# Kernel tuning notes

Measured on AMD Instinct MI355X. Metric: run time of the kernel, lower is better.

## Reference

```python
import jax, jax.numpy as jnp
import numpy as np

# Wong-Wang-Deco neural mass parameters (whobpyt defaults)
G=20.0; LAMBDA=0.0; A_E=310.0; B_E=125.0; D_E=0.16; TAU_E=100.0; W_E=1.0
A_I=615.0; B_I=177.0; D_I=0.087; TAU_I=10.0; W_I=0.7
W_PLUS=1.4; J_NMDA=0.15; J=1.0; GAMMA=0.641e-3; GAMMA_I=1.0e-3
SIG=0.01; I_0=0.382; I_EXT=0.0
DT=0.0001  # step_size
N_REGIONS=512; N_STEPS=20000


def _H(I, a, b, d, big_c):
    # firing-rate transfer function H_for_*_V3
    x = a * I - b
    numer = jnp.abs(x) + 1e-9
    neg = -d * x
    denom = jnp.where(
        neg > 50.0,
        jnp.abs(1.0 - big_c * neg) + 1e-9 * d,
        jnp.abs(1.0 - jnp.exp(jnp.minimum(neg, 51.0))) + 1e-9 * d,
    )
    return numer / denom


def setup_inputs() -> dict:
    key = jax.random.key(0)
    k1, k2, k3 = jax.random.split(key, 3)
    init_state = jax.random.uniform(k1, (N_REGIONS, 2), dtype=jnp.float32) * 0.2
    # row-normalized random structural connectivity
    Con_Mtx = jax.random.uniform(k2, (N_REGIONS, N_REGIONS), dtype=jnp.float32) / N_REGIONS
    v_of_T = jax.random.normal(k3, (N_STEPS, N_REGIONS), dtype=jnp.float32)
    return {"init_state": init_state, "Con_Mtx": Con_Mtx, "v_of_T": v_of_T}


def reference(init_state, Con_Mtx, v_of_T):
    S_E0 = init_state[:, 0]
    S_I0 = init_state[:, 1]

    def step(carry, v):
        S_E, S_I = carry
        Network_S_E = Con_Mtx @ S_E  # [N]
        I_E = W_E * I_0 + W_PLUS * J_NMDA * S_E + G * J_NMDA * Network_S_E - J * S_I + I_EXT
        I_I = W_I * I_0 + J_NMDA * S_E - S_I + LAMBDA * G * J_NMDA * Network_S_E
        r_E = _H(I_E, A_E, B_E, D_E, 1e9)
        r_I = _H(I_I, A_I, B_I, D_I, 1e5)
        dS_E = -S_E / TAU_E + (1.0 - S_E) * GAMMA * r_E + SIG * v
        dS_I = -S_I / TAU_I + GAMMA_I * r_I + SIG * v
        S_E = S_E + DT * dS_E
        S_I = S_I + DT * dS_I
        return (S_E, S_I), jnp.stack([S_E, S_I], axis=1)  # [N,2]

    (S_E, S_I), state_hist = jax.lax.scan(step, (S_E0, S_I0), v_of_T)
    state_vals = jnp.stack([S_E, S_I], axis=1)  # [N,2]
    return state_vals, state_hist  # ([N,2], [T,N,2])
```

## Files before the change

kernel.cpp:

```cpp
#include <hip/hip_runtime.h>
#include <hip/hip_bf16.h>
#include <cstdint>

#define NREG 512
#define NBLK 8
#define RPB  64
#define NTHR 512

typedef unsigned long long u64;
typedef unsigned int u32;

__device__ __forceinline__ float Hfun(float I, float a, float b, float d, float bigc) {
    float x = a * I - b;
    float numer = fabsf(x) + 1e-9f;
    float neg = -d * x;
    float denom;
    if (neg > 50.0f) {
        denom = fabsf(1.0f - bigc * neg) + 1e-9f * d;
    } else {
        denom = fabsf(1.0f - expf(fminf(neg, 51.0f))) + 1e-9f * d;
    }
    return numer / denom;
}

__global__ __launch_bounds__(NTHR, 2)
void rww_kernel(const float* __restrict__ init_state,
                const float* __restrict__ Con,
                const float* __restrict__ v_of_T,
                float* __restrict__ out,
                u64* __restrict__ xslot,
                int nsteps)
{
    __shared__ __align__(16) float sE_lds[NREG];
    __shared__ float part_lds[NTHR];

    const int tid = threadIdx.x;
    const int w   = tid >> 6;
    const int l   = tid & 63;
    const int b   = blockIdx.x;
    const int grow = b * RPB + l;

    float2* __restrict__ state2 = reinterpret_cast<float2*>(out);
    float2* __restrict__ hist2  = reinterpret_cast<float2*>(out + 2 * NREG);

    float4 cw[16];
#pragma unroll
    for (int jj = 0; jj < 16; ++jj) {
        cw[jj] = *reinterpret_cast<const float4*>(Con + (size_t)grow * NREG + w * 64 + jj * 4);
    }

    sE_lds[tid] = init_state[2 * tid];
    float sEo = 0.f, sIo = 0.f, vcur = 0.f;
    if (tid < RPB) {
        sEo  = init_state[2 * grow + 0];
        sIo  = init_state[2 * grow + 1];
        vcur = v_of_T[grow];
    }
    __syncthreads();

    for (int t = 0; t < nsteps; ++t) {
        float vnext = 0.f;
        if (tid < RPB && (t + 1) < nsteps)
            vnext = v_of_T[(size_t)(t + 1) * NREG + grow];

        const float4* s4 = reinterpret_cast<const float4*>(sE_lds) + w * 16;
        float a0 = 0.f, a1 = 0.f, a2 = 0.f, a3 = 0.f;
#pragma unroll
        for (int jj = 0; jj < 16; ++jj) {
            float4 s = s4[jj];
            a0 = fmaf(cw[jj].x, s.x, a0);
            a1 = fmaf(cw[jj].y, s.y, a1);
            a2 = fmaf(cw[jj].z, s.z, a2);
            a3 = fmaf(cw[jj].w, s.w, a3);
        }
        part_lds[w * 64 + l] = (a0 + a1) + (a2 + a3);
        __syncthreads();

        if (tid < RPB) {
            float net = 0.f;
#pragma unroll
            for (int c = 0; c < 8; ++c) net += part_lds[c * 64 + tid];

            float sE = sEo, sI = sIo;
            float I_E = 0.382f + 0.21f * sE + 3.0f * net - sI;
            float I_I = 0.2674f + 0.15f * sE - sI;
            float rE = Hfun(I_E, 310.0f, 125.0f, 0.16f, 1.0e9f);
            float rI = Hfun(I_I, 615.0f, 177.0f, 0.087f, 1.0e5f);
            float dSE = -sE * 0.01f + (1.0f - sE) * 0.000641f * rE + 0.01f * vcur;
            float dSI = -sI * 0.1f + 0.001f * rI + 0.01f * vcur;
            sEo = sE + 1e-4f * dSE;
            sIo = sI + 1e-4f * dSI;

            u64 pk = ((u64)(u32)(t + 1) << 32) | (u64)__float_as_uint(sEo);
            __hip_atomic_store(&xslot[((t + 1) & 1) * NREG + grow], pk,
                               __ATOMIC_RELAXED, __HIP_MEMORY_SCOPE_AGENT);

            hist2[(size_t)t * NREG + grow] = make_float2(sEo, sIo);
            if (t == nsteps - 1) state2[grow] = make_float2(sEo, sIo);

            vcur = vnext;
        }

        if (t + 1 < nsteps) {
            u64* slot = &xslot[((t + 1) & 1) * NREG + tid];
            const u32 want = (u32)(t + 1);
            u64 pk;
            do {
                pk = __hip_atomic_load(slot, __ATOMIC_RELAXED, __HIP_MEMORY_SCOPE_AGENT);
            } while ((u32)(pk >> 32) != want);
            sE_lds[tid] = __uint_as_float((u32)pk);
        }
        __syncthreads();
    }
}

extern "C" void kernel_launch(void* const* d_in, const int* in_sizes, int n_in,
                              void* d_out, int out_size, void* d_ws, size_t ws_size,
                              hipStream_t stream) {
    const float* init_state = (const float*)d_in[0];
    const float* Con        = (const float*)d_in[1];
    const float* v_of_T     = (const float*)d_in[2];
    int nsteps = in_sizes[2] / NREG;

    rww_kernel<<<dim3(NBLK), dim3(NTHR), 0, stream>>>(
        init_state, Con, v_of_T, (float*)d_out, (u64*)d_ws, nsteps);
}
```

Measured before the change: 32.08 ms.

## Reduce matvec via wave shuffles, double-buffer LDS state, drop one barrier per step

Each wave now owns 8 full rows and splits each row's dot product across 8 lanes. The partial sums are combined with xor shuffles, which removes the LDS partial-sum array and one block barrier per timestep. All lanes compute the nonlinearity redundantly, and the state vector is double-buffered in LDS so a single barrier suffices. Local rows are written straight to LDS instead of being polled from global, and the spin loop sleeps after repeated misses. Costs are 8x redundant transcendental work and a hand-rolled barrier that depends on correct lgkmcnt ordering.

```diff
diff --git a/kernel.cpp b/kernel.cpp
--- a/kernel.cpp
+++ b/kernel.cpp
@@ -1,10 +1,8 @@
 #include <hip/hip_runtime.h>
-#include <hip/hip_bf16.h>
 #include <cstdint>
 
 #define NREG 512
 #define NBLK 8
-#define RPB  64
 #define NTHR 512
 
 typedef unsigned long long u64;
@@ -23,7 +21,7 @@
     return numer / denom;
 }
 
-__global__ __launch_bounds__(NTHR, 2)
+__global__ __launch_bounds__(NTHR, 1)
 void rww_kernel(const float* __restrict__ init_state,
                 const float* __restrict__ Con,
                 const float* __restrict__ v_of_T,
@@ -31,86 +29,97 @@
                 u64* __restrict__ xslot,
                 int nsteps)
 {
-    __shared__ __align__(16) float sE_lds[NREG];
-    __shared__ float part_lds[NTHR];
+    __shared__ __align__(16) float buf[2][NREG];
 
     const int tid = threadIdx.x;
     const int w   = tid >> 6;
     const int l   = tid & 63;
+    const int s   = l & 7;
+    const int rl  = l >> 3;
     const int b   = blockIdx.x;
-    const int grow = b * RPB + l;
+    const int row = b * 64 + w * 8 + rl;
+    const int rot = s << 1;
 
     float2* __restrict__ state2 = reinterpret_cast<float2*>(out);
     float2* __restrict__ hist2  = reinterpret_cast<float2*>(out + 2 * NREG);
 
     float4 cw[16];
 #pragma unroll
-    for (int jj = 0; jj < 16; ++jj) {
-        cw[jj] = *reinterpret_cast<const float4*>(Con + (size_t)grow * NREG + w * 64 + jj * 4);
+    for (int k = 0; k < 16; ++k) {
+        int c = s * 64 + (((k + rot) & 15) << 2);
+        cw[k] = *reinterpret_cast<const float4*>(Con + (size_t)row * NREG + c);
     }
+#pragma unroll
+    for (int k = 0; k < 16; ++k)
+        asm volatile("" : "+v"(cw[k].x), "+v"(cw[k].y), "+v"(cw[k].z), "+v"(cw[k].w));
 
-    sE_lds[tid] = init_state[2 * tid];
-    float sEo = 0.f, sIo = 0.f, vcur = 0.f;
-    if (tid < RPB) {
-        sEo  = init_state[2 * grow + 0];
-        sIo  = init_state[2 * grow + 1];
-        vcur = v_of_T[grow];
-    }
+    buf[0][tid] = init_state[2 * tid];
+    float sEo  = init_state[2 * row];
+    float sIo  = init_state[2 * row + 1];
+    float vcur = v_of_T[row];
     __syncthreads();
 
     for (int t = 0; t < nsteps; ++t) {
         float vnext = 0.f;
-        if (tid < RPB && (t + 1) < nsteps)
-            vnext = v_of_T[(size_t)(t + 1) * NREG + grow];
+        if (t + 1 < nsteps) vnext = v_of_T[(size_t)(t + 1) * NREG + row];
 
-        const float4* s4 = reinterpret_cast<const float4*>(sE_lds) + w * 16;
+        const int p = t & 1;
+        const float* sb = &buf[p][s << 6];
         float a0 = 0.f, a1 = 0.f, a2 = 0.f, a3 = 0.f;
 #pragma unroll
-        for (int jj = 0; jj < 16; ++jj) {
-            float4 s = s4[jj];
-            a0 = fmaf(cw[jj].x, s.x, a0);
-            a1 = fmaf(cw[jj].y, s.y, a1);
-            a2 = fmaf(cw[jj].z, s.z, a2);
-            a3 = fmaf(cw[jj].w, s.w, a3);
+        for (int j = 0; j < 16; ++j) {
+            float4 sv = *reinterpret_cast<const float4*>(sb + (((j + rot) & 15) << 2));
+            a0 = fmaf(cw[j].x, sv.x, a0);
+            a1 = fmaf(cw[j].y, sv.y, a1);
+            a2 = fmaf(cw[j].z, sv.z, a2);
+            a3 = fmaf(cw[j].w, sv.w, a3);
         }
-        part_lds[w * 64 + l] = (a0 + a1) + (a2 + a3);
-        __syncthreads();
+        float net = (a0 + a1) + (a2 + a3);
+        net += __shfl_xor(net, 1, 64);
+        net += __shfl_xor(net, 2, 64);
+        net += __shfl_xor(net, 4, 64);
 
-        if (tid < RPB) {
-            float net = 0.f;
-#pragma unroll
-            for (int c = 0; c < 8; ++c) net += part_lds[c * 64 + tid];
+        float I_E = 0.382f + 0.21f * sEo + 3.0f * net - sIo;
+        float rE  = Hfun(I_E, 310.0f, 125.0f, 0.16f, 1.0e9f);
+        float dSE = -sEo * 0.01f + (1.0f - sEo) * 0.000641f * rE + 0.01f * vcur;
+        float sEn = sEo + 1e-4f * dSE;
 
-            float sE = sEo, sI = sIo;
-            float I_E = 0.382f + 0.21f * sE + 3.0f * net - sI;
-            float I_I = 0.2674f + 0.15f * sE - sI;
-            float rE = Hfun(I_E, 310.0f, 125.0f, 0.16f, 1.0e9f);
-            float rI = Hfun(I_I, 615.0f, 177.0f, 0.087f, 1.0e5f);
-            float dSE = -sE * 0.01f + (1.0f - sE) * 0.000641f * rE + 0.01f * vcur;
-            float dSI = -sI * 0.1f + 0.001f * rI + 0.01f * vcur;
-            sEo = sE + 1e-4f * dSE;
-            sIo = sI + 1e-4f * dSI;
-
-            u64 pk = ((u64)(u32)(t + 1) << 32) | (u64)__float_as_uint(sEo);
-            __hip_atomic_store(&xslot[((t + 1) & 1) * NREG + grow], pk,
+        const int pn = (t + 1) & 1;
+        u64 pk = ((u64)(u32)(t + 1) << 32) | (u64)__float_as_uint(sEn);
+        if (s == 0) {
+            __hip_atomic_store(&xslot[pn * NREG + row], pk,
                                __ATOMIC_RELAXED, __HIP_MEMORY_SCOPE_AGENT);
-
-            hist2[(size_t)t * NREG + grow] = make_float2(sEo, sIo);
-            if (t == nsteps - 1) state2[grow] = make_float2(sEo, sIo);
-
-            vcur = vnext;
+            buf[pn][row] = sEn;
         }
 
-        if (t + 1 < nsteps) {
-            u64* slot = &xslot[((t + 1) & 1) * NREG + tid];
+        float I_I = 0.2674f + 0.15f * sEo - sIo;
+        float rI  = Hfun(I_I, 615.0f, 177.0f, 0.087f, 1.0e5f);
+        float dSI = -sIo * 0.1f + 0.001f * rI + 0.01f * vcur;
+        float sIn = sIo + 1e-4f * dSI;
+        if (s == 0) {
+            hist2[(size_t)t * NREG + row] = make_float2(sEn, sIn);
+            if (t == nsteps - 1) state2[row] = make_float2(sEn, sIn);
+        }
+        sEo = sEn; sIo = sIn; vcur = vnext;
+
+        if (t + 1 < nsteps && (tid >> 6) != b) {
+            u64* slot = &xslot[pn * NREG + tid];
             const u32 want = (u32)(t + 1);
-            u64 pk;
-            do {
-                pk = __hip_atomic_load(slot, __ATOMIC_RELAXED, __HIP_MEMORY_SCOPE_AGENT);
-            } while ((u32)(pk >> 32) != want);
-            sE_lds[tid] = __uint_as_float((u32)pk);
+            u64 pk2;
+            int spins = 0;
+            for (;;) {
+                pk2 = __hip_atomic_load(slot, __ATOMIC_RELAXED, __HIP_MEMORY_SCOPE_AGENT);
+                if ((u32)(pk2 >> 32) == want) break;
+                if (++spins > 256) {
+                    __builtin_amdgcn_s_sleep(2);
+                    spins = 0;
+                }
+            }
+            buf[pn][tid] = __uint_as_float((u32)pk2);
         }
-        __syncthreads();
+
+        asm volatile("s_waitcnt lgkmcnt(0)" ::: "memory");
+        __builtin_amdgcn_s_barrier();
     }
 }
 
```

Result: slower. 33.20 ms (+3.5%).
